# Performance work log

Measured on AMD Instinct MI355X. Metric: run time of the kernel, lower is better.

The kernel has to match this reference:

```python
import jax, jax.numpy as jnp
import numpy as np

B, S, H, V = 64, 512, 1024, 32000


def setup_inputs() -> dict:
    key = jax.random.key(0)
    ks = jax.random.split(key, 20)
    sd = 0.02
    inp = {
        'x': jax.random.randint(ks[0], (B, 1), 0, V),
        'h_prev': jax.random.normal(ks[1], (B, H), dtype=jnp.float32),
        'annotations': jax.random.normal(ks[2], (B, S, H), dtype=jnp.float32),
        # embedding table
        'emb': jax.random.normal(ks[3], (V, H), dtype=jnp.float32) * sd,
        # attention MLP: Linear(2H -> H), ReLU, Linear(H -> 1)
        'attn_W1': jax.random.normal(ks[4], (H, 2 * H), dtype=jnp.float32) * sd,
        'attn_b1': jnp.zeros((H,), jnp.float32),
        'attn_W2': jax.random.normal(ks[5], (1, H), dtype=jnp.float32) * sd,
        'attn_b2': jnp.zeros((1,), jnp.float32),
        # GRU cell linears (input_size = 2H). NOTE: original code has a bug where
        # weights_hr is never used (r uses weights_hz); we replicate that, so no Whr.
        'W_ir': jax.random.normal(ks[6], (H, 2 * H), dtype=jnp.float32) * sd,
        'b_ir': jnp.zeros((H,), jnp.float32),
        'W_iz': jax.random.normal(ks[7], (H, 2 * H), dtype=jnp.float32) * sd,
        'b_iz': jnp.zeros((H,), jnp.float32),
        'W_in': jax.random.normal(ks[8], (H, 2 * H), dtype=jnp.float32) * sd,
        'b_in': jnp.zeros((H,), jnp.float32),
        'W_hz': jax.random.normal(ks[9], (H, H), dtype=jnp.float32) * sd,
        'b_hz': jnp.zeros((H,), jnp.float32),
        'W_hn': jax.random.normal(ks[10], (H, H), dtype=jnp.float32) * sd,
        'b_hn': jnp.zeros((H,), jnp.float32),
        # output projection H -> V
        'W_out': jax.random.normal(ks[11], (V, H), dtype=jnp.float32) * sd,
        'b_out': jnp.zeros((V,), jnp.float32),
    }
    return inp


def _lin(x, W, b):
    # torch nn.Linear: y = x @ W.T + b, W has shape (out, in)
    return x @ W.T + b


def reference(x, h_prev, annotations, emb, attn_W1, attn_b1, attn_W2, attn_b2,
              W_ir, b_ir, W_iz, b_iz, W_in, b_in, W_hz, b_hz, W_hn, b_hn,
              W_out, b_out):
    # embedding lookup, squeeze time dim: (B, H)
    embed = emb[x[:, 0]]

    # additive attention: concat(annotations, expanded hidden) -> MLP -> softmax
    # split W1 over the concat axis to avoid materializing the [B,S,2H] concat:
    # concat @ W1.T == annotations @ W1[:, :H].T + hidden @ W1[:, H:].T
    hA = jnp.einsum('bsh,kh->bsk', annotations, attn_W1[:, :H])  # (B,S,H)
    hB = h_prev @ attn_W1[:, H:].T                               # (B,H)
    hidden_act = jax.nn.relu(hA + hB[:, None, :] + attn_b1)
    scores = jnp.einsum('bsk,k->bs', hidden_act, attn_W2[0]) + attn_b2[0]
    attention_weights = jax.nn.softmax(scores, axis=1)[:, :, None]  # (B,S,1)

    # context vector
    context = jnp.sum(attention_weights * annotations, axis=1)  # (B,H)
    xc = jnp.concatenate([context, embed], axis=1)              # (B,2H)

    # GRU cell (faithful to the original, including the weights_hz reuse in r)
    hz = _lin(h_prev, W_hz, b_hz)
    z = jax.nn.sigmoid(_lin(xc, W_iz, b_iz) + hz)
    r = jax.nn.sigmoid(_lin(xc, W_ir, b_ir) + hz)  # bug replicated: uses W_hz
    g = jnp.tanh(_lin(xc, W_in, b_in) + r * _lin(h_prev, W_hn, b_hn))
    h_new = (1.0 - z) * g + z * h_prev

    output = _lin(h_new, W_out, b_out)  # (B,V)
    return output, h_new, attention_weights
```

## Files before the change

### kernel.cpp

```cpp
#include <hip/hip_runtime.h>


typedef __bf16 bf16;
typedef __attribute__((ext_vector_type(4))) float  f32x4;
typedef __attribute__((ext_vector_type(4))) float  fx4;
typedef __attribute__((ext_vector_type(8))) bf16   bf16x8;
typedef __attribute__((ext_vector_type(4))) bf16   bf16x4;
typedef __attribute__((ext_vector_type(4))) unsigned int u32x4;
typedef __attribute__((ext_vector_type(2))) unsigned int u32x2;

#define MFMA16x16x32(a, b, c) __builtin_amdgcn_mfma_f32_16x16x32_bf16(a, b, c, 0, 0, 0)

#define Bb   64
#define Ss   512
#define Hh   1024
#define Vv   32000
#define Mtot (Bb * Ss)

#define WS_HNEW_B    131072
#define WS_XC_B      262144
#define WS_W1A_B     524288
#define WS_P_HB      2621440
#define WS_P_HZ      3670016
#define WS_P_HN      4718592
#define WS_P_IZ      5767168
#define WS_P_IR      6815744
#define WS_P_IN      7864320
#define WS_SCORES    8912896
#define WS_CTX       11010048
#define WS_ANNB      13107200

#define OUT_LOGITS   0
#define OUT_HNEW     2048000
#define OUT_AW       2113536

__device__ __forceinline__ float bf2f(unsigned short u) {
    unsigned int x = ((unsigned int)u) << 16;
    float f;
    __builtin_memcpy(&f, &x, 4);
    return f;
}

__device__ __forceinline__ void gload_lds16(const bf16* g, bf16* l)
{
    __builtin_amdgcn_global_load_lds(
        (const __attribute__((address_space(1))) unsigned int*)g,
        (__attribute__((address_space(3))) unsigned int*)l,
        16, 0, 0);
}

__global__ __launch_bounds__(256, 2) void k_pre(
    const int* __restrict__ x, const float* __restrict__ h_prev,
    const float* __restrict__ emb, const float* __restrict__ attn_W1,
    const float* __restrict__ W_hz, const float* __restrict__ W_hn,
    const float* __restrict__ ann,
    bf16* __restrict__ xc_b, bf16* __restrict__ W1a_b, bf16* __restrict__ annb,
    float* __restrict__ p_hB, float* __restrict__ p_hz, float* __restrict__ p_hn)
{
    __shared__ __align__(16) bf16 lA[2][64][72];
    __shared__ __align__(16) bf16 lB[2][64][72];

    int bid = blockIdx.x, t = threadIdx.x;

    if (bid >= 1280) {
        size_t i = ((size_t)(bid - 1280) * 256 + t) * 8;
        size_t stride = (size_t)2048 * 256 * 8;
        size_t n = (size_t)Mtot * Hh;
        for (; i < n; i += stride) {
            fx4 v0 = *(const fx4*)(ann + i);
            fx4 v1 = *(const fx4*)(ann + i + 4);
            bf16x8 o;
#pragma unroll
            for (int q = 0; q < 4; q++) { o[q] = (bf16)v0[q]; o[q + 4] = (bf16)v1[q]; }
            *(bf16x8*)(annb + i) = o;
        }
        return;
    }
    if (bid >= 192) {
        int sub = bid - 192;
        if (sub < 64) {
            int b = sub, row = x[b];
            for (int i = t; i < Hh; i += 256)
                xc_b[b * 2048 + Hh + i] = (bf16)emb[(size_t)row * Hh + i];
        } else {
            int row = sub - 64;
            int k4 = t * 4;
            fx4 v = *(const fx4*)(attn_W1 + (size_t)row * 2048 + k4);
            bf16x4 o;
#pragma unroll
            for (int q = 0; q < 4; q++) o[q] = (bf16)v[q];
            *(bf16x4*)(W1a_b + (size_t)row * Hh + k4) = o;
        }
        return;
    }

    int nb = bid & 15, sk = (bid >> 4) & 3, mat = bid >> 6;
    const float* Bp = (mat == 0) ? (attn_W1 + 1024) : (mat == 1 ? W_hz : W_hn);
    int ldb         = (mat == 0) ? 2048 : 1024;
    float* op       = (mat == 0) ? p_hB : (mat == 1 ? p_hz : p_hn);

    int n0 = nb * 64, k0 = sk * 256;
    int lane = t & 63, wid = t >> 6;
    int srow = t >> 2, schunk = t & 3;

    const float* agp = h_prev + (size_t)srow * 1024 + k0 + schunk * 16;
    const float* bgp = Bp + (size_t)(n0 + srow) * ldb + k0 + schunk * 16;

    f32x4 acc[4];
#pragma unroll
    for (int i = 0; i < 4; i++) acc[i] = (f32x4)0.0f;

    fx4 aRf[4], bRf[4];
#pragma unroll
    for (int q = 0; q < 4; q++) { aRf[q] = *(const fx4*)(agp + q * 4);
                                  bRf[q] = *(const fx4*)(bgp + q * 4); }
    {
        bf16x8 a0, a1, p0, p1;
#pragma unroll
        for (int q = 0; q < 4; q++) {
            a0[q] = (bf16)aRf[0][q]; a0[q + 4] = (bf16)aRf[1][q];
            a1[q] = (bf16)aRf[2][q]; a1[q + 4] = (bf16)aRf[3][q];
            p0[q] = (bf16)bRf[0][q]; p0[q + 4] = (bf16)bRf[1][q];
            p1[q] = (bf16)bRf[2][q]; p1[q + 4] = (bf16)bRf[3][q];
        }
        *(bf16x8*)&lA[0][srow][schunk * 16]     = a0;
        *(bf16x8*)&lA[0][srow][schunk * 16 + 8] = a1;
        *(bf16x8*)&lB[0][srow][schunk * 16]     = p0;
        *(bf16x8*)&lB[0][srow][schunk * 16 + 8] = p1;
    }
    __syncthreads();

    int cur = 0;
    for (int ks = 0; ks < 4; ks++) {
        if (ks + 1 < 4) {
#pragma unroll
            for (int q = 0; q < 4; q++) {
                aRf[q] = *(const fx4*)(agp + (ks + 1) * 64 + q * 4);
                bRf[q] = *(const fx4*)(bgp + (ks + 1) * 64 + q * 4);
            }
        }
        int rA = lane & 15;
        int kc = (lane >> 4) * 8;
#pragma unroll
        for (int kk = 0; kk < 2; kk++) {
            bf16x8 bfr = *(bf16x8*)&lB[cur][wid * 16 + rA][kk * 32 + kc];
#pragma unroll
            for (int i = 0; i < 4; i++) {
                bf16x8 af = *(bf16x8*)&lA[cur][i * 16 + rA][kk * 32 + kc];
                acc[i] = MFMA16x16x32(af, bfr, acc[i]);
            }
        }
        if (ks + 1 < 4) {
            int nxt = cur ^ 1;
            bf16x8 a0, a1, p0, p1;
#pragma unroll
            for (int q = 0; q < 4; q++) {
                a0[q] = (bf16)aRf[0][q]; a0[q + 4] = (bf16)aRf[1][q];
                a1[q] = (bf16)aRf[2][q]; a1[q + 4] = (bf16)aRf[3][q];
                p0[q] = (bf16)bRf[0][q]; p0[q + 4] = (bf16)bRf[1][q];
                p1[q] = (bf16)bRf[2][q]; p1[q + 4] = (bf16)bRf[3][q];
            }
            *(bf16x8*)&lA[nxt][srow][schunk * 16]     = a0;
            *(bf16x8*)&lA[nxt][srow][schunk * 16 + 8] = a1;
            *(bf16x8*)&lB[nxt][srow][schunk * 16]     = p0;
            *(bf16x8*)&lB[nxt][srow][schunk * 16 + 8] = p1;
        }
        __syncthreads();
        cur ^= 1;
    }

    int n = n0 + wid * 16 + (lane & 15);
#pragma unroll
    for (int i = 0; i < 4; i++)
#pragma unroll
        for (int r = 0; r < 4; r++) {
            int m = i * 16 + (lane >> 4) * 4 + r;
            op[(size_t)(sk * 64 + m) * 1024 + n] = acc[i][r];
        }
}

__global__ __launch_bounds__(256, 2) void k_sgemm(
    const bf16* __restrict__ A, int lda, int kchunk,
    const float* __restrict__ B0, const float* __restrict__ B1, const float* __restrict__ B2,
    int ldb0, int ldb1, int ldb2,
    float* __restrict__ o0, float* __restrict__ o1, float* __restrict__ o2,
    const float* __restrict__ bias, int N, int finalOut)
{
    __shared__ __align__(16) bf16 lA[2][64][72];
    __shared__ __align__(16) bf16 lB[2][64][72];

    int nb = blockIdx.x, sk = blockIdx.y, mat = blockIdx.z;
    const float* Bp = (mat == 0) ? B0 : (mat == 1 ? B1 : B2);
    int ldb         = (mat == 0) ? ldb0 : (mat == 1 ? ldb1 : ldb2);
    float* op       = (mat == 0) ? o0 : (mat == 1 ? o1 : o2);

    int n0 = nb * 64, k0 = sk * kchunk;
    int t = threadIdx.x, lane = t & 63, wid = t >> 6;
    int srow = t >> 2, schunk = t & 3;

    const bf16*  agp = A  + (size_t)srow * lda + k0 + schunk * 16;
    const float* bgp = Bp + (size_t)(n0 + srow) * ldb + k0 + schunk * 16;

    f32x4 acc[4];
#pragma unroll
    for (int i = 0; i < 4; i++) acc[i] = (f32x4)0.0f;

    u32x4 aR0, aR1; fx4 bRf[4];
    int nk = kchunk >> 6;

    aR0 = *(const u32x4*)(agp);
    aR1 = *(const u32x4*)(agp + 8);
#pragma unroll
    for (int q = 0; q < 4; q++) bRf[q] = *(const fx4*)(bgp + q * 4);
    {
        *(u32x4*)&lA[0][srow][schunk * 16]     = aR0;
        *(u32x4*)&lA[0][srow][schunk * 16 + 8] = aR1;
        bf16x8 p0, p1;
#pragma unroll
        for (int q = 0; q < 4; q++) {
            p0[q] = (bf16)bRf[0][q]; p0[q + 4] = (bf16)bRf[1][q];
            p1[q] = (bf16)bRf[2][q]; p1[q + 4] = (bf16)bRf[3][q];
        }
        *(bf16x8*)&lB[0][srow][schunk * 16]     = p0;
        *(bf16x8*)&lB[0][srow][schunk * 16 + 8] = p1;
    }
    __syncthreads();

    int cur = 0;
    for (int ks = 0; ks < nk; ks++) {
        if (ks + 1 < nk) {
            aR0 = *(const u32x4*)(agp + (ks + 1) * 64);
            aR1 = *(const u32x4*)(agp + (ks + 1) * 64 + 8);
#pragma unroll
            for (int q = 0; q < 4; q++) bRf[q] = *(const fx4*)(bgp + (ks + 1) * 64 + q * 4);
        }
        int rA = lane & 15;
        int kc = (lane >> 4) * 8;
#pragma unroll
        for (int kk = 0; kk < 2; kk++) {
            bf16x8 bfr = *(bf16x8*)&lB[cur][wid * 16 + rA][kk * 32 + kc];
#pragma unroll
            for (int i = 0; i < 4; i++) {
                bf16x8 af = *(bf16x8*)&lA[cur][i * 16 + rA][kk * 32 + kc];
                acc[i] = MFMA16x16x32(af, bfr, acc[i]);
            }
        }
        if (ks + 1 < nk) {
            int nxt = cur ^ 1;
            *(u32x4*)&lA[nxt][srow][schunk * 16]     = aR0;
            *(u32x4*)&lA[nxt][srow][schunk * 16 + 8] = aR1;
            bf16x8 p0, p1;
#pragma unroll
            for (int q = 0; q < 4; q++) {
                p0[q] = (bf16)bRf[0][q]; p0[q + 4] = (bf16)bRf[1][q];
                p1[q] = (bf16)bRf[2][q]; p1[q + 4] = (bf16)bRf[3][q];
            }
            *(bf16x8*)&lB[nxt][srow][schunk * 16]     = p0;
            *(bf16x8*)&lB[nxt][srow][schunk * 16 + 8] = p1;
        }
        __syncthreads();
        cur ^= 1;
    }

    int n = n0 + wid * 16 + (lane & 15);
#pragma unroll
    for (int i = 0; i < 4; i++) {
#pragma unroll
        for (int r = 0; r < 4; r++) {
            int m = i * 16 + (lane >> 4) * 4 + r;
            float v = acc[i][r];
            if (finalOut) op[(size_t)m * N + n] = v + bias[n];
            else          op[(size_t)(sk * 64 + m) * N + n] = v;
        }
    }
}

__global__ __launch_bounds__(512, 2) void k_attn(
    const bf16* __restrict__ annb, const bf16* __restrict__ Bw,
    const float* __restrict__ p_hB, const float* __restrict__ b1,
    const float* __restrict__ W2, float* __restrict__ scores_part)
{
    extern __shared__ char smem[];

    int bid = blockIdx.x;
    int wgid = (bid & 7) * 64 + (bid >> 3);
    int mb = wgid >> 2, nbp = wgid & 3;

    int t = threadIdx.x, lane = t & 63, wid = t >> 6;
    int wm = wid >> 2, wn = wid & 3;
    int r = lane & 15, q = lane >> 4;

    int srow = t >> 3;
    int gc   = (t & 7) ^ (srow & 7);
    size_t goff = (size_t)srow * 1024 + gc * 8;
    int doff = wid * 1024;
    const bf16* aSrc = annb + (size_t)mb * 262144;
    const bf16* bSrc = Bw   + (size_t)nbp * 262144;

    int e0 = (q ^ (r & 7)) * 16, e1 = e0 ^ 64;
    int rowAoff = (wm * 64 + r) * 128;
    int rowBoff = 32768 + (wn * 32 + r) * 128;

#define STAGEOP(src, half, buf, mat, kt) do {                                  \
        const bf16* s_ = (src) + (half) * 131072 + (size_t)(kt) * 64 + goff;   \
        char* d_ = smem + (buf) * 65536 + (mat) * 32768 + (half) * 16384 + doff; \
        gload_lds16(s_, (bf16*)d_);                                            \
        gload_lds16(s_ + 65536, (bf16*)(d_ + 8192));                           \
    } while (0)

#define VMW(n) asm volatile("s_waitcnt vmcnt(" #n ")" ::: "memory")

    f32x4 acc[8][4];
#pragma unroll
    for (int i = 0; i < 8; i++)
#pragma unroll
        for (int j = 0; j < 4; j++) acc[i][j] = (f32x4)0.0f;

    bf16x8 aq[4][2], bq[2][2];

#define PHASE(IH, JH, RA, RB, STG, WAITQ) do {                                 \
        if (RA) {                                                              \
            _Pragma("unroll")                                                  \
            for (int ip = 0; ip < 4; ip++) {                                   \
                const char* pa_ = smem + cur * 65536 + (IH) * 16384            \
                                + rowAoff + ip * 2048;                         \
                aq[ip][0] = *(const bf16x8*)(pa_ + e0);                        \
                aq[ip][1] = *(const bf16x8*)(pa_ + e1);                        \
            }                                                                  \
        }                                                                      \
        if (RB) {                                                              \
            _Pragma("unroll")                                                  \
            for (int jp = 0; jp < 2; jp++) {                                   \
                const char* pb_ = smem + cur * 65536 + (JH) * 16384            \
                                + rowBoff + jp * 2048;                         \
                bq[jp][0] = *(const bf16x8*)(pb_ + e0);                        \
                bq[jp][1] = *(const bf16x8*)(pb_ + e1);                        \
            }                                                                  \
        }                                                                      \
        STG;                                                                   \
        __builtin_amdgcn_s_barrier();                                          \
        __builtin_amdgcn_s_setprio(1);                                         \
        _Pragma("unroll")                                                      \
        for (int ip = 0; ip < 4; ip++)                                         \
            _Pragma("unroll")                                                  \
            for (int jp = 0; jp < 2; jp++)                                     \
                _Pragma("unroll")                                              \
                for (int ks = 0; ks < 2; ks++)                                 \
                    acc[(IH) * 4 + ip][(JH) * 2 + jp] =                        \
                        MFMA16x16x32(aq[ip][ks], bq[jp][ks],                   \
                                     acc[(IH) * 4 + ip][(JH) * 2 + jp]);       \
        __builtin_amdgcn_s_setprio(0);                                         \
        WAITQ;                                                                 \
        __builtin_amdgcn_s_barrier();                                          \
    } while (0)

    STAGEOP(aSrc, 0, 0, 0, 0);
    STAGEOP(bSrc, 0, 0, 1, 0);
    STAGEOP(aSrc, 1, 0, 0, 0);
    STAGEOP(bSrc, 1, 0, 1, 0);
    VMW(0);
    __builtin_amdgcn_s_barrier();

#pragma unroll 1
    for (int kt = 0; kt < 15; kt++) {
        int cur = kt & 1, nxt = cur ^ 1;
        PHASE(0, 0, 1, 1, { STAGEOP(aSrc, 0, nxt, 0, kt + 1);
                            STAGEOP(bSrc, 0, nxt, 1, kt + 1); }, VMW(6));
        PHASE(1, 0, 1, 0, { STAGEOP(aSrc, 1, nxt, 0, kt + 1); }, VMW(6));
        PHASE(1, 1, 0, 1, , (void)0);
        PHASE(0, 1, 1, 0, { STAGEOP(bSrc, 1, nxt, 1, kt + 1); }, VMW(4));
    }
    {
        int cur = 1;
        PHASE(0, 0, 1, 1, , VMW(2));
        PHASE(1, 0, 1, 0, , VMW(0));
        PHASE(1, 1, 0, 1, , (void)0);
        PHASE(0, 1, 1, 0, , (void)0);
    }
#undef PHASE
#undef STAGEOP

    int m0 = mb * 256, n0g = nbp * 256;
    int b = m0 >> 9;
    float hb[4], w2v[4];
#pragma unroll
    for (int j = 0; j < 4; j++) {
        int n = n0g + (j >> 1) * 128 + wn * 32 + (j & 1) * 16 + r;
        float h = p_hB[b * Hh + n] + p_hB[65536 + b * Hh + n]
                + p_hB[131072 + b * Hh + n] + p_hB[196608 + b * Hh + n];
        hb[j]  = h + b1[n];
        w2v[j] = W2[n];
    }
    float red[32];
#pragma unroll
    for (int i = 0; i < 8; i++)
#pragma unroll
        for (int rr = 0; rr < 4; rr++) {
            float s = 0.f;
#pragma unroll
            for (int j = 0; j < 4; j++) {
                float v = acc[i][j][rr] + hb[j];
                v = fmaxf(v, 0.f);
                s += v * w2v[j];
            }
            red[i * 4 + rr] = s;
        }
#pragma unroll
    for (int mask = 1; mask <= 8; mask <<= 1)
#pragma unroll
        for (int p = 0; p < 32; p++)
            red[p] += __shfl_xor(red[p], mask, 64);

    if (r == 0) {
        float* sp = scores_part + (size_t)(nbp * 4 + wn) * Mtot;
#pragma unroll
        for (int i = 0; i < 8; i++) {
            int m = m0 + wm * 64 + (i & 3) * 16 + (i >> 2) * 128 + q * 4;
#pragma unroll
            for (int rr = 0; rr < 4; rr++)
                sp[m + rr] = red[i * 4 + rr];
        }
    }
}

__global__ void k_softmax(const float* __restrict__ scores_part, float* __restrict__ aw)
{
    int b = blockIdx.x, s = threadIdx.x;
    int lane = s & 63, wid = s >> 6;
    float v = 0.f;
#pragma unroll
    for (int p = 0; p < 16; p++) v += scores_part[(size_t)p * Mtot + b * Ss + s];

    __shared__ float redm[8], redsum[8];
    float m = v;
#pragma unroll
    for (int mask = 32; mask; mask >>= 1) m = fmaxf(m, __shfl_xor(m, mask, 64));
    if (lane == 0) redm[wid] = m;
    __syncthreads();
    float bm = redm[0];
#pragma unroll
    for (int w = 1; w < 8; w++) bm = fmaxf(bm, redm[w]);

    float e = expf(v - bm);
    float ss = e;
#pragma unroll
    for (int mask = 32; mask; mask >>= 1) ss += __shfl_xor(ss, mask, 64);
    if (lane == 0) redsum[wid] = ss;
    __syncthreads();
    float tot = 0.f;
#pragma unroll
    for (int w = 0; w < 8; w++) tot += redsum[w];

    aw[b * Ss + s] = e / tot;
}

__global__ void k_context(const bf16* __restrict__ annb, const float* __restrict__ aw,
                          float* __restrict__ ctx_part)
{
    __shared__ float law[64];
    int bid = blockIdx.x;
    int b = bid >> 3, sc = bid & 7;
    int t = threadIdx.x;
    if (t < 64) law[t] = aw[b * Ss + sc * 64 + t];
    __syncthreads();
    int h0 = t * 4;
    const bf16* ap = annb + (size_t)(b * Ss + sc * 64) * Hh + h0;
    float a0 = 0, a1 = 0, a2 = 0, a3 = 0;
#pragma unroll 4
    for (int s2 = 0; s2 < 64; s2++) {
        float w = law[s2];
        u32x2 v = *(const u32x2*)(ap + (size_t)s2 * Hh);
        a0 += w * bf2f((unsigned short)(v[0] & 0xffff));
        a1 += w * bf2f((unsigned short)(v[0] >> 16));
        a2 += w * bf2f((unsigned short)(v[1] & 0xffff));
        a3 += w * bf2f((unsigned short)(v[1] >> 16));
    }
    fx4 o; o[0] = a0; o[1] = a1; o[2] = a2; o[3] = a3;
    *(fx4*)(ctx_part + sc * 65536 + b * Hh + h0) = o;
}

__global__ void k_xc(const float* __restrict__ ctx_part, bf16* __restrict__ xc_b)
{
    int idx = blockIdx.x * 256 + threadIdx.x;
    float c = 0.f;
#pragma unroll
    for (int p = 0; p < 8; p++) c += ctx_part[p * 65536 + idx];
    int b = idx >> 10, h = idx & 1023;
    xc_b[b * 2048 + h] = (bf16)c;
}

__global__ void k_gru(const float* __restrict__ p_iz, const float* __restrict__ p_ir,
                      const float* __restrict__ p_in, const float* __restrict__ p_hz,
                      const float* __restrict__ p_hn,
                      const float* __restrict__ b_iz, const float* __restrict__ b_ir,
                      const float* __restrict__ b_in, const float* __restrict__ b_hz,
                      const float* __restrict__ b_hn,
                      const float* __restrict__ h_prev,
                      float* __restrict__ out_h, bf16* __restrict__ h_new_b)
{
    int idx = blockIdx.x * 256 + threadIdx.x;
    int o = idx & 1023;
    float iz = p_iz[idx] + p_iz[65536 + idx] + p_iz[131072 + idx] + p_iz[196608 + idx];
    float ir = p_ir[idx] + p_ir[65536 + idx] + p_ir[131072 + idx] + p_ir[196608 + idx];
    float in_ = p_in[idx] + p_in[65536 + idx] + p_in[131072 + idx] + p_in[196608 + idx];
    float hz = p_hz[idx] + p_hz[65536 + idx] + p_hz[131072 + idx] + p_hz[196608 + idx];
    float hn = p_hn[idx] + p_hn[65536 + idx] + p_hn[131072 + idx] + p_hn[196608 + idx];
    hz += b_hz[o];
    hn += b_hn[o];
    float z = 1.f / (1.f + expf(-(iz + b_iz[o] + hz)));
    float r = 1.f / (1.f + expf(-(ir + b_ir[o] + hz)));
    float g = tanhf(in_ + b_in[o] + r * hn);
    float hp = h_prev[idx];
    float hnew = (1.f - z) * g + z * hp;
    out_h[idx] = hnew;
    h_new_b[idx] = (bf16)hnew;
}

extern "C" void kernel_launch(void* const* d_in, const int* in_sizes, int n_in,
                              void* d_out, int out_size, void* d_ws, size_t ws_size,
                              hipStream_t stream)
{
    const int*   x        = (const int*)d_in[0];
    const float* h_prev   = (const float*)d_in[1];
    const float* ann      = (const float*)d_in[2];
    const float* emb      = (const float*)d_in[3];
    const float* attn_W1  = (const float*)d_in[4];
    const float* attn_b1  = (const float*)d_in[5];
    const float* attn_W2  = (const float*)d_in[6];
    const float* W_ir     = (const float*)d_in[8];
    const float* b_ir     = (const float*)d_in[9];
    const float* W_iz     = (const float*)d_in[10];
    const float* b_iz     = (const float*)d_in[11];
    const float* W_in     = (const float*)d_in[12];
    const float* b_in     = (const float*)d_in[13];
    const float* W_hz     = (const float*)d_in[14];
    const float* b_hz     = (const float*)d_in[15];
    const float* W_hn     = (const float*)d_in[16];
    const float* b_hn     = (const float*)d_in[17];
    const float* W_out    = (const float*)d_in[18];
    const float* b_out    = (const float*)d_in[19];

    float* out = (float*)d_out;
    char*  ws  = (char*)d_ws;

    bf16*  h_new_b  = (bf16*)(ws + WS_HNEW_B);
    bf16*  xc_b     = (bf16*)(ws + WS_XC_B);
    bf16*  W1a_b    = (bf16*)(ws + WS_W1A_B);
    float* p_hB     = (float*)(ws + WS_P_HB);
    float* p_hz     = (float*)(ws + WS_P_HZ);
    float* p_hn     = (float*)(ws + WS_P_HN);
    float* p_iz     = (float*)(ws + WS_P_IZ);
    float* p_ir     = (float*)(ws + WS_P_IR);
    float* p_in     = (float*)(ws + WS_P_IN);
    float* scores_p = (float*)(ws + WS_SCORES);
    float* ctx_part = (float*)(ws + WS_CTX);
    bf16*  annb     = (bf16*)(ws + WS_ANNB);

    hipFuncSetAttribute(reinterpret_cast<const void*>(k_attn),
                        hipFuncAttributeMaxDynamicSharedMemorySize, 131072);

    k_pre<<<3328, 256, 0, stream>>>(x, h_prev, emb, attn_W1, W_hz, W_hn, ann,
                                    xc_b, W1a_b, annb, p_hB, p_hz, p_hn);

    k_attn<<<512, 512, 131072, stream>>>(annb, W1a_b, p_hB, attn_b1, attn_W2,
                                         scores_p);

    k_softmax<<<64, 512, 0, stream>>>(scores_p, out + OUT_AW);

    k_context<<<512, 256, 0, stream>>>(annb, out + OUT_AW, ctx_part);

    k_xc<<<256, 256, 0, stream>>>(ctx_part, xc_b);

    {
        dim3 g(16, 4, 3);
        k_sgemm<<<g, 256, 0, stream>>>(xc_b, 2048, 512,
                                       W_iz, W_ir, W_in, 2048, 2048, 2048,
                                       p_iz, p_ir, p_in, nullptr, 1024, 0);
    }

    k_gru<<<256, 256, 0, stream>>>(p_iz, p_ir, p_in, p_hz, p_hn,
                                   b_iz, b_ir, b_in, b_hz, b_hn,
                                   h_prev, out + OUT_HNEW, h_new_b);

    {
        dim3 g(500, 1, 1);
        k_sgemm<<<g, 256, 0, stream>>>(h_new_b, 1024, 1024,
                                       W_out, W_out, W_out, 1024, 1024, 1024,
                                       out + OUT_LOGITS, nullptr, nullptr,
                                       b_out, 32000, 1);
    }
}
```

Before: 171.3 us.

## Load attention A operand straight from global into registers, stage only B in LDS

The attention GEMM kernel no longer stages the annotation (A) tiles through shared memory. Each wave now loads its A fragments directly from global memory into registers, double-buffered across k-steps, and only the W1 (B) tiles go through LDS. Dynamic shared memory drops from 128 KB to 64 KB and the per-phase barriers collapse to one per k-step. The cost is more live registers, uncoalesced-style per-lane global loads and reliance on vmcnt ordering for correctness.

New measurement: 237.6 us. 38.7% more time.

```diff
diff --git a/kernel.cpp b/kernel.cpp
--- a/kernel.cpp
+++ b/kernel.cpp
@@ -277,7 +277,7 @@
 
 __global__ __launch_bounds__(512, 2) void k_attn(
     const bf16* __restrict__ annb, const bf16* __restrict__ Bw,
-    const float* __restrict__ p_hB, const float* __restrict__ b1,
+    const float* __restrict__ p_hB, const float* __restrict__ b1v,
     const float* __restrict__ W2, float* __restrict__ scores_part)
 {
     extern __shared__ char smem[];
@@ -291,54 +291,42 @@
     int r = lane & 15, q = lane >> 4;
 
     int srow = t >> 3;
-    int gc   = (t & 7) ^ (srow & 7);
+    int gc = (t & 7) ^ (srow & 7);
     size_t goff = (size_t)srow * 1024 + gc * 8;
     int doff = wid * 1024;
-    const bf16* aSrc = annb + (size_t)mb * 262144;
-    const bf16* bSrc = Bw   + (size_t)nbp * 262144;
-
-    int e0 = (q ^ (r & 7)) * 16, e1 = e0 ^ 64;
-    int rowAoff = (wm * 64 + r) * 128;
-    int rowBoff = 32768 + (wn * 32 + r) * 128;
-
-#define STAGEOP(src, half, buf, mat, kt) do {                                  \
-        const bf16* s_ = (src) + (half) * 131072 + (size_t)(kt) * 64 + goff;   \
-        char* d_ = smem + (buf) * 65536 + (mat) * 32768 + (half) * 16384 + doff; \
+    const bf16* bSrc = Bw + (size_t)nbp * 262144;
+
+#define BSTAGE(half, buf, kt) do {                                             \
+        const bf16* s_ = bSrc + (half) * 131072 + (size_t)(kt) * 64 + goff;    \
+        char* d_ = smem + (buf) * 32768 + (half) * 16384 + doff;               \
         gload_lds16(s_, (bf16*)d_);                                            \
         gload_lds16(s_ + 65536, (bf16*)(d_ + 8192));                           \
     } while (0)
 
-#define VMW(n) asm volatile("s_waitcnt vmcnt(" #n ")" ::: "memory")
-
-    f32x4 acc[8][4];
-#pragma unroll
-    for (int i = 0; i < 8; i++)
-#pragma unroll
-        for (int j = 0; j < 4; j++) acc[i][j] = (f32x4)0.0f;
-
-    bf16x8 aq[4][2], bq[2][2];
-
-#define PHASE(IH, JH, RA, RB, STG, WAITQ) do {                                 \
-        if (RA) {                                                              \
-            _Pragma("unroll")                                                  \
-            for (int ip = 0; ip < 4; ip++) {                                   \
-                const char* pa_ = smem + cur * 65536 + (IH) * 16384            \
-                                + rowAoff + ip * 2048;                         \
-                aq[ip][0] = *(const bf16x8*)(pa_ + e0);                        \
-                aq[ip][1] = *(const bf16x8*)(pa_ + e1);                        \
-            }                                                                  \
+    int e0 = (q ^ (r & 7)) * 16, e1 = e0 ^ 64;
+
+#define BREAD(dst, jh, bufb) do {                                              \
+        _Pragma("unroll")                                                      \
+        for (int jp = 0; jp < 2; jp++) {                                       \
+            const char* pb_ = smem + (bufb) + (jh) * 16384                     \
+                            + (wn * 32 + jp * 16 + r) * 128;                   \
+            dst[jp * 2 + 0] = *(const bf16x8*)(pb_ + e0);                      \
+            dst[jp * 2 + 1] = *(const bf16x8*)(pb_ + e1);                      \
         }                                                                      \
-        if (RB) {                                                              \
-            _Pragma("unroll")                                                  \
-            for (int jp = 0; jp < 2; jp++) {                                   \
-                const char* pb_ = smem + cur * 65536 + (JH) * 16384            \
-                                + rowBoff + jp * 2048;                         \
-                bq[jp][0] = *(const bf16x8*)(pb_ + e0);                        \
-                bq[jp][1] = *(const bf16x8*)(pb_ + e1);                        \
-            }                                                                  \
+    } while (0)
+
+    const bf16* aG = annb + (size_t)(mb * 256 + wm * 64 + r) * 1024 + q * 8;
+
+#define ALOAD(dst, ih, kt) do {                                                \
+        _Pragma("unroll")                                                      \
+        for (int ip = 0; ip < 4; ip++) {                                       \
+            const bf16* p_ = aG + (ih) * 131072 + ip * 16384 + (size_t)(kt) * 64; \
+            dst[ip * 2 + 0] = *(const bf16x8*)(p_);                            \
+            dst[ip * 2 + 1] = *(const bf16x8*)(p_ + 32);                       \
         }                                                                      \
-        STG;                                                                   \
-        __builtin_amdgcn_s_barrier();                                          \
+    } while (0)
+
+#define MM(IH, JH, aqv, bqv) do {                                              \
         __builtin_amdgcn_s_setprio(1);                                         \
         _Pragma("unroll")                                                      \
         for (int ip = 0; ip < 4; ip++)                                         \
@@ -347,38 +335,53 @@
                 _Pragma("unroll")                                              \
                 for (int ks = 0; ks < 2; ks++)                                 \
                     acc[(IH) * 4 + ip][(JH) * 2 + jp] =                        \
-                        MFMA16x16x32(aq[ip][ks], bq[jp][ks],                   \
+                        MFMA16x16x32(aqv[ip * 2 + ks], bqv[jp * 2 + ks],       \
                                      acc[(IH) * 4 + ip][(JH) * 2 + jp]);       \
         __builtin_amdgcn_s_setprio(0);                                         \
-        WAITQ;                                                                 \
-        __builtin_amdgcn_s_barrier();                                          \
     } while (0)
 
-    STAGEOP(aSrc, 0, 0, 0, 0);
-    STAGEOP(bSrc, 0, 0, 1, 0);
-    STAGEOP(aSrc, 1, 0, 0, 0);
-    STAGEOP(bSrc, 1, 0, 1, 0);
-    VMW(0);
+    f32x4 acc[8][4];
+#pragma unroll
+    for (int i = 0; i < 8; i++)
+#pragma unroll
+        for (int j = 0; j < 4; j++) acc[i][j] = (f32x4)0.0f;
+
+    bf16x8 aqc[8], aqn[8], bq0[4], bq1[4];
+
+    BSTAGE(0, 0, 0);
+    BSTAGE(1, 0, 0);
+    ALOAD(aqc, 0, 0);
+    __builtin_amdgcn_sched_barrier(0);
+    asm volatile("s_waitcnt vmcnt(8)" ::: "memory");
     __builtin_amdgcn_s_barrier();
 
 #pragma unroll 1
-    for (int kt = 0; kt < 15; kt++) {
-        int cur = kt & 1, nxt = cur ^ 1;
-        PHASE(0, 0, 1, 1, { STAGEOP(aSrc, 0, nxt, 0, kt + 1);
-                            STAGEOP(bSrc, 0, nxt, 1, kt + 1); }, VMW(6));
-        PHASE(1, 0, 1, 0, { STAGEOP(aSrc, 1, nxt, 0, kt + 1); }, VMW(6));
-        PHASE(1, 1, 0, 1, , (void)0);
-        PHASE(0, 1, 1, 0, { STAGEOP(bSrc, 1, nxt, 1, kt + 1); }, VMW(4));
-    }
-    {
-        int cur = 1;
-        PHASE(0, 0, 1, 1, , VMW(2));
-        PHASE(1, 0, 1, 0, , VMW(0));
-        PHASE(1, 1, 0, 1, , (void)0);
-        PHASE(0, 1, 1, 0, , (void)0);
-    }
-#undef PHASE
-#undef STAGEOP
+    for (int kt = 0; kt < 16; kt++) {
+        int curb = (kt & 1) * 32768, nxtb = curb ^ 32768;
+
+        if (kt < 15) { BSTAGE(0, (kt & 1) ^ 1, kt + 1);
+                       BSTAGE(1, (kt & 1) ^ 1, kt + 1); }
+        __builtin_amdgcn_sched_barrier(0);
+
+        BREAD(bq0, 0, curb);
+        ALOAD(aqn, 1, kt);
+        MM(0, 0, aqc, bq0);
+
+        BREAD(bq1, 1, curb);
+        MM(0, 1, aqc, bq1);
+
+        if (kt < 15) ALOAD(aqc, 0, kt + 1);
+        MM(1, 1, aqn, bq1);
+        MM(1, 0, aqn, bq0);
+
+        __builtin_amdgcn_sched_barrier(0);
+        asm volatile("s_waitcnt vmcnt(8)" ::: "memory");
+        __builtin_amdgcn_s_barrier();
+    }
+#undef MM
+#undef ALOAD
+#undef BREAD
+#undef BSTAGE
 
     int m0 = mb * 256, n0g = nbp * 256;
     int b = m0 >> 9;
@@ -388,7 +391,7 @@
         int n = n0g + (j >> 1) * 128 + wn * 32 + (j & 1) * 16 + r;
         float h = p_hB[b * Hh + n] + p_hB[65536 + b * Hh + n]
                 + p_hB[131072 + b * Hh + n] + p_hB[196608 + b * Hh + n];
-        hb[j]  = h + b1[n];
+        hb[j]  = h + b1v[n];
         w2v[j] = W2[n];
     }
     float red[32];
@@ -556,14 +559,14 @@
     float* ctx_part = (float*)(ws + WS_CTX);
     bf16*  annb     = (bf16*)(ws + WS_ANNB);
 
-    hipFuncSetAttribute(reinterpret_cast<const void*>(k_attn),
-                        hipFuncAttributeMaxDynamicSharedMemorySize, 131072);
+    (void)hipFuncSetAttribute(reinterpret_cast<const void*>(k_attn),
+                              hipFuncAttributeMaxDynamicSharedMemorySize, 131072);
 
     k_pre<<<3328, 256, 0, stream>>>(x, h_prev, emb, attn_W1, W_hz, W_hn, ann,
                                     xc_b, W1a_b, annb, p_hB, p_hz, p_hn);
 
-    k_attn<<<512, 512, 131072, stream>>>(annb, W1a_b, p_hB, attn_b1, attn_W2,
-                                         scores_p);
+    k_attn<<<512, 512, 65536, stream>>>(annb, W1a_b, p_hB, attn_b1, attn_W2,
+                                        scores_p);
 
     k_softmax<<<64, 512, 0, stream>>>(scores_p, out + OUT_AW);
 
```
